# Kernel optimization log

Hardware: AMD Instinct MI355X
Metric: run time of the kernel (lower is better)

Reference implementation:

```python
import jax, jax.numpy as jnp
import numpy as np

N_HEADS = 8
TANH_CLIP = 10.0
NEG = -1e9  # finite stand-in for -inf so log_softmax/vjp stay NaN-free


def setup_inputs() -> dict:
    key = jax.random.key(0)
    ks = jax.random.split(key, 8)
    B, N, D = 256, 1000, 128
    embeddings = jax.random.normal(ks[0], (B, N, D), dtype=jnp.float32)
    W_node = jax.random.normal(ks[1], (D, 3 * D), dtype=jnp.float32) * (1.0 / np.sqrt(D))
    W_fixed = jax.random.normal(ks[2], (D, D), dtype=jnp.float32) * (1.0 / np.sqrt(D))
    W_step = jax.random.normal(ks[3], (2 * D, D), dtype=jnp.float32) * (1.0 / np.sqrt(2 * D))
    W_out = jax.random.normal(ks[4], (D, D), dtype=jnp.float32) * (1.0 / np.sqrt(D))
    first_idx = jax.random.randint(ks[5], (B,), 0, N)
    last_idx = jax.random.randint(ks[6], (B,), 0, N)
    mask = jax.random.randint(ks[7], (B, N), 0, 2).astype(jnp.bool_)
    mask = mask.at[:, 0].set(False)  # guarantee at least one feasible node
    return {"embeddings": embeddings, "W_node": W_node, "W_fixed": W_fixed,
            "W_step": W_step, "W_out": W_out, "first_idx": first_idx,
            "last_idx": last_idx, "mask": mask}


def reference(embeddings, W_node, W_fixed, W_step, W_out, first_idx, last_idx, mask):
    # One pointer-network decode step (TSP variant of AttentionModel._get_log_p),
    # including the _precompute projections.
    B, N, D = embeddings.shape
    H = N_HEADS
    dk = D // H

    # _precompute: fixed context + glimpse K/V + logit key
    graph_embed = embeddings.mean(axis=1)                       # [B, D]
    fixed_ctx = graph_embed @ W_fixed                           # [B, D]
    kvl = embeddings @ W_node                                   # [B, N, 3D]
    K, V, logit_K = jnp.split(kvl, 3, axis=-1)                  # each [B, N, D]

    # step context: cat(first-node emb, last-node emb) -> project to D
    b = jnp.arange(B)
    step_ctx = jnp.concatenate([embeddings[b, first_idx], embeddings[b, last_idx]], axis=-1)  # [B, 2D]
    q = fixed_ctx + step_ctx @ W_step                           # [B, D]

    # masked multi-head glimpse attention (q_len = 1)
    qh = q.reshape(B, H, dk)                                    # [B, H, dk]
    Kh = K.reshape(B, N, H, dk)
    Vh = V.reshape(B, N, H, dk)
    compat = jnp.einsum('bhd,bnhd->bhn', qh, Kh) / np.sqrt(dk)  # [B, H, N]
    compat = jnp.where(mask[:, None, :], NEG, compat)           # mask_inner
    attn = jax.nn.softmax(compat, axis=-1)
    heads = jnp.einsum('bhn,bnhd->bhd', attn, Vh)               # [B, H, dk]
    glimpse = heads.reshape(B, D) @ W_out                       # [B, D]

    # single-head logit attention with tanh clipping
    logits = jnp.einsum('bd,bnd->bn', glimpse, logit_K) / np.sqrt(D)  # [B, N]
    logits = jnp.tanh(logits) * TANH_CLIP
    logits = jnp.where(mask, NEG, logits)                       # mask_logits
    return jax.nn.log_softmax(logits, axis=-1)                  # [B, N]
```

## Files before the change

kernel.cpp:

```cpp
#include <hip/hip_runtime.h>


#define NEG (-1e9f)

__global__ __launch_bounds__(1024) void k_fused(
    const float* __restrict__ E, const float* __restrict__ Wn,
    const float* __restrict__ Wf, const float* __restrict__ Ws,
    const float* __restrict__ Wo,
    const int* __restrict__ fi, const int* __restrict__ li,
    const int* __restrict__ maskI, const unsigned char* __restrict__ maskB,
    float* __restrict__ out)
{
    const int b = blockIdx.x;
    const int t = threadIdx.x;

    __shared__ float4 Et[4096];
    __shared__ float4 qk4[256];
    __shared__ float4 pt4[256];
    __shared__ float4 EbarF4[256];
    __shared__ float4 mu4[32], e14[32], e24[32], gp4[32];
    __shared__ float q[128], heads[128], gl[128];
    __shared__ float qred[8][128];
    __shared__ float ct[128 * 9];
    __shared__ float redh[72];
    __shared__ float mh[8], lh[8], al[8];
    __shared__ float red[16];
    __shared__ float stat[2];
    __shared__ int flagS;

    float* const mu = (float*)mu4;
    float* const e1 = (float*)e14;
    float* const e2 = (float*)e24;
    float* const gp = (float*)gp4;
    float* const pt = (float*)pt4;
    float* const EbarF = (float*)EbarF4;
    float* const qkf = (float*)qk4;

    const float4* E4 = (const float4*)(E + (size_t)b * 128000);

    if (t == 0) flagS = 0;
    const uint4 dv = ((const uint4*)maskI)[t];
    const unsigned det = (dv.x | dv.y | dv.z | dv.w) & 0xFFFFFF00u;

    {
        const int cm = t & 31, sm = t >> 5;
        float4 acc = make_float4(0.f, 0.f, 0.f, 0.f);
        for (int r = sm; r < 1000; r += 32) {
            const float4 v = E4[r * 32 + cm];
            acc.x += v.x; acc.y += v.y; acc.z += v.z; acc.w += v.w;
        }
        Et[t] = acc;
    }
    if (t >= 512 && t < 544) {
        e14[t - 512] = E4[fi[b] * 32 + (t - 512)];
    } else if (t >= 544 && t < 576) {
        e24[t - 544] = E4[li[b] * 32 + (t - 544)];
    }
    __syncthreads();
    if (det) atomicOr(&flagS, 1);
    if (t < 32) {
        float4 acc = Et[t];
        #pragma unroll
        for (int s = 1; s < 32; ++s) {
            const float4 v = Et[s * 32 + t];
            acc.x += v.x; acc.y += v.y; acc.z += v.z; acc.w += v.w;
        }
        const float inv = 1.0f / 1000.0f;
        mu4[t] = make_float4(acc.x * inv, acc.y * inv, acc.z * inv, acc.w * inv);
    }
    __syncthreads();

    {
        const int part = t >> 7, d = t & 127;
        float acc = 0.f;
        const int k0 = part * 48;
        for (int k = k0; k < k0 + 48; ++k) {
            const float s = (k < 128) ? mu[k] : (k < 256 ? e1[k - 128] : e2[k - 256]);
            const float w = (k < 128) ? Wf[k * 128 + d] : Ws[(k - 128) * 128 + d];
            acc += s * w;
        }
        qred[part][d] = acc;
    }
    __syncthreads();
    if (t < 128) {
        float acc = 0.f;
        #pragma unroll
        for (int p = 0; p < 8; ++p) acc += qred[p][t];
        q[t] = acc;
    }
    __syncthreads();
    {
        const int j = t & 127, cg = t >> 7;
        const float qj = q[j];
        for (int c0 = 0; c0 < 128; c0 += 8) {
            const int c = c0 + cg;
            float v = Wn[c * 384 + j] * qj;
            v += __shfl_down(v, 8, 16);
            v += __shfl_down(v, 4, 16);
            v += __shfl_down(v, 2, 16);
            v += __shfl_down(v, 1, 16);
            if ((j & 15) == 0) {
                const int h = j >> 4, s = c >> 2;
                qkf[h * 128 + (s ^ (s >> 2)) * 4 + (c & 3)] = v * 0.25f;
            }
        }
    }
    __syncthreads();

    const bool useB = (flagS != 0);

    if (t < 8) { mh[t] = -3e38f; lh[t] = 0.f; }
    float4 eacc[8];
    #pragma unroll
    for (int h = 0; h < 8; ++h) eacc[h] = make_float4(0.f, 0.f, 0.f, 0.f);
    const int c4 = t & 31, sl = t >> 5;
    const int rr = t >> 3, qq = t & 7;

    for (int tile = 0; tile < 8; ++tile) {
        const int r0 = tile * 128;
        {
            const int g = r0 + rr;
            float4 v[4];
            if (g < 1000) {
                #pragma unroll
                for (int i = 0; i < 4; ++i) v[i] = E4[g * 32 + qq * 4 + i];
            } else {
                #pragma unroll
                for (int i = 0; i < 4; ++i) v[i] = make_float4(0.f, 0.f, 0.f, 0.f);
            }
            float pch[8];
            #pragma unroll
            for (int h = 0; h < 8; ++h) pch[h] = 0.f;
            #pragma unroll
            for (int i = 0; i < 4; ++i) {
                const int grp = qq * 4 + i;
                Et[rr * 32 + (grp ^ (rr & 7))] = v[i];
                const int sg = grp ^ (grp >> 2);
                #pragma unroll
                for (int h = 0; h < 8; ++h) {
                    const float4 w = qk4[h * 32 + sg];
                    pch[h] += v[i].x * w.x + v[i].y * w.y + v[i].z * w.z + v[i].w * w.w;
                }
            }
            #pragma unroll
            for (int m = 1; m <= 4; m <<= 1) {
                #pragma unroll
                for (int h = 0; h < 8; ++h) pch[h] += __shfl_xor(pch[h], m, 64);
            }
            bool msk = (g >= 1000);
            if (!msk) msk = useB ? (maskB[b * 1000 + g] != 0)
                                 : (maskI[b * 1000 + g] != 0);
            ct[rr * 9 + qq] = msk ? NEG : pch[qq];
        }
        __syncthreads();
        if (t < 64) {
            const int h = t & 7, part = t >> 3;
            float mt = -3e38f;
            const int rb = part * 16;
            for (int r = 0; r < 16; ++r) mt = fmaxf(mt, ct[(rb + r) * 9 + h]);
            redh[part * 9 + h] = mt;
        }
        __syncthreads();
        if (t < 8) {
            float mt = redh[t];
            for (int p = 1; p < 8; ++p) mt = fmaxf(mt, redh[p * 9 + t]);
            const float mnew = fmaxf(mh[t], mt);
            al[t] = __expf(mh[t] - mnew);
            mh[t] = mnew;
        }
        __syncthreads();
        {
            const int row = t >> 3, h = t & 7;
            pt[row * 8 + h] = __expf(ct[row * 9 + h] - mh[h]);
        }
        __syncthreads();
        {
            #pragma unroll
            for (int h = 0; h < 8; ++h) {
                const float a = al[h];
                eacc[h].x *= a; eacc[h].y *= a; eacc[h].z *= a; eacc[h].w *= a;
            }
            #pragma unroll
            for (int j = 0; j < 4; ++j) {
                const int r = sl * 4 + j;
                const float4 ev = Et[r * 32 + (c4 ^ (r & 7))];
                const float4 p0 = pt4[r * 2];
                const float4 p1 = pt4[r * 2 + 1];
                eacc[0].x += p0.x * ev.x; eacc[0].y += p0.x * ev.y; eacc[0].z += p0.x * ev.z; eacc[0].w += p0.x * ev.w;
                eacc[1].x += p0.y * ev.x; eacc[1].y += p0.y * ev.y; eacc[1].z += p0.y * ev.z; eacc[1].w += p0.y * ev.w;
                eacc[2].x += p0.z * ev.x; eacc[2].y += p0.z * ev.y; eacc[2].z += p0.z * ev.z; eacc[2].w += p0.z * ev.w;
                eacc[3].x += p0.w * ev.x; eacc[3].y += p0.w * ev.y; eacc[3].z += p0.w * ev.z; eacc[3].w += p0.w * ev.w;
                eacc[4].x += p1.x * ev.x; eacc[4].y += p1.x * ev.y; eacc[4].z += p1.x * ev.z; eacc[4].w += p1.x * ev.w;
                eacc[5].x += p1.y * ev.x; eacc[5].y += p1.y * ev.y; eacc[5].z += p1.y * ev.z; eacc[5].w += p1.y * ev.w;
                eacc[6].x += p1.z * ev.x; eacc[6].y += p1.z * ev.y; eacc[6].z += p1.z * ev.z; eacc[6].w += p1.z * ev.w;
                eacc[7].x += p1.w * ev.x; eacc[7].y += p1.w * ev.y; eacc[7].z += p1.w * ev.z; eacc[7].w += p1.w * ev.w;
            }
        }
        if (t < 64) {
            const int h = t & 7, part = t >> 3;
            float s = 0.f;
            const int rb = part * 16;
            for (int r = 0; r < 16; ++r) s += pt[(rb + r) * 8 + h];
            redh[part * 9 + h] = s;
        }
        __syncthreads();
        if (t < 8) {
            float s = 0.f;
            for (int p = 0; p < 8; ++p) s += redh[p * 9 + t];
            lh[t] = lh[t] * al[t] + s;
        }
    }

    if (sl >= 16) {
        #pragma unroll
        for (int h = 0; h < 8; ++h) Et[(sl - 16) * 256 + h * 32 + c4] = eacc[h];
    }
    __syncthreads();
    if (sl < 16) {
        #pragma unroll
        for (int h = 0; h < 8; ++h) {
            const float4 o = Et[sl * 256 + h * 32 + c4];
            eacc[h].x += o.x; eacc[h].y += o.y; eacc[h].z += o.z; eacc[h].w += o.w;
            Et[sl * 256 + h * 32 + c4] = eacc[h];
        }
    }
    __syncthreads();
    if (t < 256) {
        const int h = t >> 5, cc = t & 31;
        float4 s = make_float4(0.f, 0.f, 0.f, 0.f);
        #pragma unroll
        for (int s2 = 0; s2 < 16; ++s2) {
            const float4 v = Et[s2 * 256 + h * 32 + cc];
            s.x += v.x; s.y += v.y; s.z += v.z; s.w += v.w;
        }
        const float invl = 1.0f / lh[h];
        EbarF4[h * 32 + cc] = make_float4(s.x * invl, s.y * invl, s.z * invl, s.w * invl);
    }
    __syncthreads();

    {
        const int part = t >> 7, d = t & 127, h = d >> 4;
        float acc = 0.f;
        const int c0 = part * 16;
        for (int c = c0; c < c0 + 16; ++c) acc += EbarF[h * 128 + c] * Wn[c * 384 + 128 + d];
        qred[part][d] = acc;
    }
    __syncthreads();
    if (t < 128) {
        float acc = 0.f;
        #pragma unroll
        for (int p = 0; p < 8; ++p) acc += qred[p][t];
        heads[t] = acc;
    }
    __syncthreads();
    {
        const int part = t >> 7, d = t & 127;
        float acc = 0.f;
        const int j0 = part * 16;
        for (int j = j0; j < j0 + 16; ++j) acc += heads[j] * Wo[j * 128 + d];
        qred[part][d] = acc;
    }
    __syncthreads();
    if (t < 128) {
        float acc = 0.f;
        #pragma unroll
        for (int p = 0; p < 8; ++p) acc += qred[p][t];
        gl[t] = acc;
    }
    __syncthreads();
    {
        const int part = t >> 7, c = t & 127;
        float acc = 0.f;
        const int d0 = part * 16;
        for (int d = d0; d < d0 + 16; ++d) acc += Wn[c * 384 + 256 + d] * gl[d];
        qred[part][c] = acc;
    }
    __syncthreads();
    if (t < 128) {
        float acc = 0.f;
        #pragma unroll
        for (int p = 0; p < 8; ++p) acc += qred[p][t];
        gp[t] = acc * 0.08838834764831845f;
    }
    __syncthreads();

    {
        const int row = t >> 3, sub = t & 7;
        for (int tile = 0; tile < 8; ++tile) {
            const int g = tile * 128 + row;
            float acc = 0.f;
            if (g < 1000) {
                #pragma unroll
                for (int i = 0; i < 4; ++i) {
                    const float4 v = E4[g * 32 + sub * 4 + i];
                    const float4 w = gp4[sub * 4 + i];
                    acc += v.x * w.x + v.y * w.y + v.z * w.z + v.w * w.w;
                }
            }
            ct[row * 9 + sub] = acc;
            __syncthreads();
            if (t < 128) {
                const int g2 = tile * 128 + t;
                if (g2 < 1000) {
                    float s = 0.f;
                    #pragma unroll
                    for (int k = 0; k < 8; ++k) s += ct[t * 9 + k];
                    float zz = 10.0f * tanhf(s);
                    const bool m = useB ? (maskB[b * 1000 + g2] != 0)
                                        : (maskI[b * 1000 + g2] != 0);
                    if (m) zz = NEG;
                    pt[g2] = zz;
                }
            }
            __syncthreads();
        }
    }
    float v = (t < 1000) ? pt[t] : -3e38f;
    #pragma unroll
    for (int off = 32; off > 0; off >>= 1) v = fmaxf(v, __shfl_down(v, off, 64));
    if ((t & 63) == 0) red[t >> 6] = v;
    __syncthreads();
    if (t == 0) {
        float m = red[0];
        for (int i = 1; i < 16; ++i) m = fmaxf(m, red[i]);
        stat[0] = m;
    }
    __syncthreads();
    float sv = (t < 1000) ? __expf(pt[t] - stat[0]) : 0.f;
    #pragma unroll
    for (int off = 32; off > 0; off >>= 1) sv += __shfl_down(sv, off, 64);
    if ((t & 63) == 0) red[t >> 6] = sv;
    __syncthreads();
    if (t == 0) {
        float s = 0.f;
        for (int i = 0; i < 16; ++i) s += red[i];
        stat[1] = stat[0] + __logf(s);
    }
    __syncthreads();
    if (t < 1000)
        out[(size_t)b * 1000 + t] = pt[t] - stat[1];
}

extern "C" void kernel_launch(void* const* d_in, const int* in_sizes, int n_in,
                              void* d_out, int out_size, void* d_ws, size_t ws_size,
                              hipStream_t stream) {
    const float* E  = (const float*)d_in[0];
    const float* Wn = (const float*)d_in[1];
    const float* Wf = (const float*)d_in[2];
    const float* Ws = (const float*)d_in[3];
    const float* Wo = (const float*)d_in[4];
    const int*   fi = (const int*)d_in[5];
    const int*   li = (const int*)d_in[6];
    const int*   maskI = (const int*)d_in[7];
    const unsigned char* maskB = (const unsigned char*)d_in[7];
    float* out = (float*)d_out;

    k_fused<<<256, 1024, 0, stream>>>(E, Wn, Wf, Ws, Wo, fi, li, maskI, maskB, out);
}
```

Baseline: 284.4 us.

## Split each batch row across two blocks with pairwise global-memory sync

Launches 512 blocks cooperatively, with each pair of blocks handling half of the 1000 nodes for one batch element. Partial mean, attention-softmax state and log-sum-exp statistics are exchanged through workspace memory using an atomic counter barrier per pair. The goal is to double the number of blocks so that 256 CUs are filled better and per-block latency drops. In exchange it adds three spin-wait barriers, a memset, and extra workspace traffic, and it depends on both blocks of a pair being resident at once. It also relayouts the attention-value accumulation to scalar per-column accumulators over a smaller tile.

Result: slower. 725.2 us (+154.9%).

```diff
diff --git a/kernel.cpp b/kernel.cpp
--- a/kernel.cpp
+++ b/kernel.cpp
@@ -3,20 +3,42 @@
 
 #define NEG (-1e9f)
 
-__global__ __launch_bounds__(1024) void k_fused(
+__device__ __forceinline__ void pair_sync(int* c, int target) {
+    __syncthreads();
+    if (threadIdx.x == 0) {
+        __hip_atomic_fetch_add(c, 1, __ATOMIC_RELEASE, __HIP_MEMORY_SCOPE_AGENT);
+        while (__hip_atomic_load(c, __ATOMIC_RELAXED, __HIP_MEMORY_SCOPE_AGENT) < target)
+            __builtin_amdgcn_s_sleep(4);
+        __threadfence();
+    }
+    __syncthreads();
+}
+
+__global__ __launch_bounds__(1024, 8) void k_fused(
     const float* __restrict__ E, const float* __restrict__ Wn,
     const float* __restrict__ Wf, const float* __restrict__ Ws,
     const float* __restrict__ Wo,
     const int* __restrict__ fi, const int* __restrict__ li,
     const int* __restrict__ maskI, const unsigned char* __restrict__ maskB,
-    float* __restrict__ out)
+    float* __restrict__ out, float* __restrict__ ws)
 {
-    const int b = blockIdx.x;
-    const int t = threadIdx.x;
-
-    __shared__ float4 Et[4096];
+    const int bid  = blockIdx.x;
+    const int b    = bid & 255;
+    const int half = bid >> 8;
+    const int blk  = b * 2 + half;
+    const int i0   = b * 2, i1 = b * 2 + 1;
+    const int t    = threadIdx.x;
+    const int r0g  = half * 500;
+
+    int*   cnt  = (int*)ws;
+    float* muP  = ws + 256;
+    float* wsU  = muP + 512 * 128;
+    float* wsML = wsU + (size_t)512 * 1024;
+    float* wsZ  = wsML + 512 * 16;
+
+    __shared__ float4 Et4[2048];
     __shared__ float4 qk4[256];
-    __shared__ float4 pt4[256];
+    __shared__ float4 pt4[128];
     __shared__ float4 EbarF4[256];
     __shared__ float4 mu4[32], e14[32], e24[32], gp4[32];
     __shared__ float q[128], heads[128], gl[128];
@@ -28,13 +50,14 @@
     __shared__ float stat[2];
     __shared__ int flagS;
 
-    float* const mu = (float*)mu4;
-    float* const e1 = (float*)e14;
-    float* const e2 = (float*)e24;
-    float* const gp = (float*)gp4;
-    float* const pt = (float*)pt4;
+    float* const mu    = (float*)mu4;
+    float* const e1    = (float*)e14;
+    float* const e2    = (float*)e24;
+    float* const gp    = (float*)gp4;
+    float* const pt    = (float*)pt4;
     float* const EbarF = (float*)EbarF4;
-    float* const qkf = (float*)qk4;
+    float* const qkf   = (float*)qk4;
+    float* const Etf   = (float*)Et4;
 
     const float4* E4 = (const float4*)(E + (size_t)b * 128000);
 
@@ -45,11 +68,11 @@
     {
         const int cm = t & 31, sm = t >> 5;
         float4 acc = make_float4(0.f, 0.f, 0.f, 0.f);
-        for (int r = sm; r < 1000; r += 32) {
-            const float4 v = E4[r * 32 + cm];
+        for (int r = sm; r < 500; r += 32) {
+            const float4 v = E4[(r0g + r) * 32 + cm];
             acc.x += v.x; acc.y += v.y; acc.z += v.z; acc.w += v.w;
         }
-        Et[t] = acc;
+        Et4[t] = acc;
     }
     if (t >= 512 && t < 544) {
         e14[t - 512] = E4[fi[b] * 32 + (t - 512)];
@@ -59,14 +82,21 @@
     __syncthreads();
     if (det) atomicOr(&flagS, 1);
     if (t < 32) {
-        float4 acc = Et[t];
+        float4 acc = Et4[t];
         #pragma unroll
         for (int s = 1; s < 32; ++s) {
-            const float4 v = Et[s * 32 + t];
+            const float4 v = Et4[s * 32 + t];
             acc.x += v.x; acc.y += v.y; acc.z += v.z; acc.w += v.w;
         }
+        ((float4*)(muP + (size_t)blk * 128))[t] = acc;
+    }
+    pair_sync(&cnt[b], 2);
+    if (t < 32) {
+        const float4 p0 = ((const float4*)(muP + (size_t)i0 * 128))[t];
+        const float4 p1 = ((const float4*)(muP + (size_t)i1 * 128))[t];
         const float inv = 1.0f / 1000.0f;
-        mu4[t] = make_float4(acc.x * inv, acc.y * inv, acc.z * inv, acc.w * inv);
+        mu4[t] = make_float4((p0.x + p1.x) * inv, (p0.y + p1.y) * inv,
+                             (p0.z + p1.z) * inv, (p0.w + p1.w) * inv);
     }
     __syncthreads();
 
@@ -110,131 +140,126 @@
     const bool useB = (flagS != 0);
 
     if (t < 8) { mh[t] = -3e38f; lh[t] = 0.f; }
-    float4 eacc[8];
+    float eacc[8];
     #pragma unroll
-    for (int h = 0; h < 8; ++h) eacc[h] = make_float4(0.f, 0.f, 0.f, 0.f);
-    const int c4 = t & 31, sl = t >> 5;
-    const int rr = t >> 3, qq = t & 7;
+    for (int h = 0; h < 8; ++h) eacc[h] = 0.f;
+    const int rr = t >> 4, qq = t & 15;
+    const int esl = t >> 7, ec = t & 127;
+    const int g1 = qq, g2 = qq + 16;
+    const int sg1 = g1 ^ (g1 >> 2), sg2 = g2 ^ (g2 >> 2);
 
     for (int tile = 0; tile < 8; ++tile) {
-        const int r0 = tile * 128;
+        const int lr = tile * 64 + rr;
+        const bool valid = (lr < 500);
         {
-            const int g = r0 + rr;
-            float4 v[4];
-            if (g < 1000) {
+            float4 v0 = make_float4(0.f, 0.f, 0.f, 0.f), v1 = v0;
+            if (valid) {
+                v0 = E4[(r0g + lr) * 32 + g1];
+                v1 = E4[(r0g + lr) * 32 + g2];
+            }
+            bool msk = !valid;
+            if (valid && qq < 8)
+                msk = useB ? (maskB[b * 1000 + r0g + lr] != 0)
+                           : (maskI[b * 1000 + r0g + lr] != 0);
+            Et4[rr * 32 + g1] = v0;
+            Et4[rr * 32 + g2] = v1;
+            float pch[8];
+            #pragma unroll
+            for (int h = 0; h < 8; ++h) {
+                const float4 w0 = qk4[h * 32 + sg1];
+                const float4 w1 = qk4[h * 32 + sg2];
+                pch[h] = v0.x * w0.x + v0.y * w0.y + v0.z * w0.z + v0.w * w0.w
+                       + v1.x * w1.x + v1.y * w1.y + v1.z * w1.z + v1.w * w1.w;
+            }
+            #pragma unroll
+            for (int m = 1; m <= 8; m <<= 1) {
                 #pragma unroll
-                for (int i = 0; i < 4; ++i) v[i] = E4[g * 32 + qq * 4 + i];
-            } else {
-                #pragma unroll
-                for (int i = 0; i < 4; ++i) v[i] = make_float4(0.f, 0.f, 0.f, 0.f);
-            }
-            float pch[8];
-            #pragma unroll
-            for (int h = 0; h < 8; ++h) pch[h] = 0.f;
-            #pragma unroll
-            for (int i = 0; i < 4; ++i) {
-                const int grp = qq * 4 + i;
-                Et[rr * 32 + (grp ^ (rr & 7))] = v[i];
-                const int sg = grp ^ (grp >> 2);
-                #pragma unroll
-                for (int h = 0; h < 8; ++h) {
-                    const float4 w = qk4[h * 32 + sg];
-                    pch[h] += v[i].x * w.x + v[i].y * w.y + v[i].z * w.z + v[i].w * w.w;
-                }
-            }
-            #pragma unroll
-            for (int m = 1; m <= 4; m <<= 1) {
-                #pragma unroll
-                for (int h = 0; h < 8; ++h) pch[h] += __shfl_xor(pch[h], m, 64);
-            }
-            bool msk = (g >= 1000);
-            if (!msk) msk = useB ? (maskB[b * 1000 + g] != 0)
-                                 : (maskI[b * 1000 + g] != 0);
-            ct[rr * 9 + qq] = msk ? NEG : pch[qq];
+                for (int h = 0; h < 8; ++h) pch[h] += __shfl_xor(pch[h], m, 16);
+            }
+            if (qq < 8) ct[rr * 9 + qq] = msk ? NEG : pch[qq];
         }
         __syncthreads();
         if (t < 64) {
             const int h = t & 7, part = t >> 3;
             float mt = -3e38f;
-            const int rb = part * 16;
-            for (int r = 0; r < 16; ++r) mt = fmaxf(mt, ct[(rb + r) * 9 + h]);
+            const int rb = part * 8;
+            #pragma unroll
+            for (int r = 0; r < 8; ++r) mt = fmaxf(mt, ct[(rb + r) * 9 + h]);
             redh[part * 9 + h] = mt;
         }
         __syncthreads();
         if (t < 8) {
             float mt = redh[t];
+            #pragma unroll
             for (int p = 1; p < 8; ++p) mt = fmaxf(mt, redh[p * 9 + t]);
             const float mnew = fmaxf(mh[t], mt);
             al[t] = __expf(mh[t] - mnew);
             mh[t] = mnew;
         }
         __syncthreads();
-        {
+        if (t < 512) {
             const int row = t >> 3, h = t & 7;
             pt[row * 8 + h] = __expf(ct[row * 9 + h] - mh[h]);
         }
         __syncthreads();
         {
             #pragma unroll
-            for (int h = 0; h < 8; ++h) {
-                const float a = al[h];
-                eacc[h].x *= a; eacc[h].y *= a; eacc[h].z *= a; eacc[h].w *= a;
-            }
-            #pragma unroll
-            for (int j = 0; j < 4; ++j) {
-                const int r = sl * 4 + j;
-                const float4 ev = Et[r * 32 + (c4 ^ (r & 7))];
+            for (int h = 0; h < 8; ++h) eacc[h] *= al[h];
+            #pragma unroll
+            for (int j = 0; j < 8; ++j) {
+                const int r = esl * 8 + j;
+                const float ev = Etf[r * 128 + ec];
                 const float4 p0 = pt4[r * 2];
                 const float4 p1 = pt4[r * 2 + 1];
-                eacc[0].x += p0.x * ev.x; eacc[0].y += p0.x * ev.y; eacc[0].z += p0.x * ev.z; eacc[0].w += p0.x * ev.w;
-                eacc[1].x += p0.y * ev.x; eacc[1].y += p0.y * ev.y; eacc[1].z += p0.y * ev.z; eacc[1].w += p0.y * ev.w;
-                eacc[2].x += p0.z * ev.x; eacc[2].y += p0.z * ev.y; eacc[2].z += p0.z * ev.z; eacc[2].w += p0.z * ev.w;
-                eacc[3].x += p0.w * ev.x; eacc[3].y += p0.w * ev.y; eacc[3].z += p0.w * ev.z; eacc[3].w += p0.w * ev.w;
-                eacc[4].x += p1.x * ev.x; eacc[4].y += p1.x * ev.y; eacc[4].z += p1.x * ev.z; eacc[4].w += p1.x * ev.w;
-                eacc[5].x += p1.y * ev.x; eacc[5].y += p1.y * ev.y; eacc[5].z += p1.y * ev.z; eacc[5].w += p1.y * ev.w;
-                eacc[6].x += p1.z * ev.x; eacc[6].y += p1.z * ev.y; eacc[6].z += p1.z * ev.z; eacc[6].w += p1.z * ev.w;
-                eacc[7].x += p1.w * ev.x; eacc[7].y += p1.w * ev.y; eacc[7].z += p1.w * ev.z; eacc[7].w += p1.w * ev.w;
+                eacc[0] += p0.x * ev; eacc[1] += p0.y * ev;
+                eacc[2] += p0.z * ev; eacc[3] += p0.w * ev;
+                eacc[4] += p1.x * ev; eacc[5] += p1.y * ev;
+                eacc[6] += p1.z * ev; eacc[7] += p1.w * ev;
             }
         }
         if (t < 64) {
             const int h = t & 7, part = t >> 3;
             float s = 0.f;
-            const int rb = part * 16;
-            for (int r = 0; r < 16; ++r) s += pt[(rb + r) * 8 + h];
+            const int rb = part * 8;
+            #pragma unroll
+            for (int r = 0; r < 8; ++r) s += pt[(rb + r) * 8 + h];
             redh[part * 9 + h] = s;
         }
         __syncthreads();
         if (t < 8) {
             float s = 0.f;
+            #pragma unroll
             for (int p = 0; p < 8; ++p) s += redh[p * 9 + t];
             lh[t] = lh[t] * al[t] + s;
         }
     }
 
-    if (sl >= 16) {
-        #pragma unroll
-        for (int h = 0; h < 8; ++h) Et[(sl - 16) * 256 + h * 32 + c4] = eacc[h];
-    }
-    __syncthreads();
-    if (sl < 16) {
-        #pragma unroll
-        for (int h = 0; h < 8; ++h) {
-            const float4 o = Et[sl * 256 + h * 32 + c4];
-            eacc[h].x += o.x; eacc[h].y += o.y; eacc[h].z += o.z; eacc[h].w += o.w;
-            Et[sl * 256 + h * 32 + c4] = eacc[h];
-        }
-    }
-    __syncthreads();
-    if (t < 256) {
-        const int h = t >> 5, cc = t & 31;
-        float4 s = make_float4(0.f, 0.f, 0.f, 0.f);
-        #pragma unroll
-        for (int s2 = 0; s2 < 16; ++s2) {
-            const float4 v = Et[s2 * 256 + h * 32 + cc];
-            s.x += v.x; s.y += v.y; s.z += v.z; s.w += v.w;
-        }
-        const float invl = 1.0f / lh[h];
-        EbarF4[h * 32 + cc] = make_float4(s.x * invl, s.y * invl, s.z * invl, s.w * invl);
+    #pragma unroll
+    for (int h = 0; h < 8; ++h) Etf[esl * 1024 + h * 128 + ec] = eacc[h];
+    __syncthreads();
+    {
+        float s = 0.f;
+        #pragma unroll
+        for (int s2 = 0; s2 < 8; ++s2) s += Etf[s2 * 1024 + t];
+        wsU[(size_t)blk * 1024 + t] = s;
+    }
+    if (t < 8) wsML[blk * 16 + t] = mh[t];
+    else if (t < 16) wsML[blk * 16 + t] = lh[t - 8];
+    pair_sync(&cnt[b], 4);
+    if (t < 8) {
+        const float m0 = wsML[i0 * 16 + t], m1 = wsML[i1 * 16 + t];
+        const float l0 = wsML[i0 * 16 + 8 + t], l1 = wsML[i1 * 16 + 8 + t];
+        const float M = fmaxf(m0, m1);
+        const float w0 = __expf(m0 - M), w1 = __expf(m1 - M);
+        const float L = l0 * w0 + l1 * w1;
+        redh[t] = w0 / L;
+        redh[8 + t] = w1 / L;
+    }
+    __syncthreads();
+    {
+        const int h = t >> 7;
+        EbarF[t] = wsU[(size_t)i0 * 1024 + t] * redh[h]
+                 + wsU[(size_t)i1 * 1024 + t] * redh[8 + h];
     }
     __syncthreads();
 
@@ -286,10 +311,11 @@
 
     {
         const int row = t >> 3, sub = t & 7;
-        for (int tile = 0; tile < 8; ++tile) {
-            const int g = tile * 128 + row;
+        for (int tile = 0; tile < 4; ++tile) {
+            const int lr = tile * 128 + row;
             float acc = 0.f;
-            if (g < 1000) {
+            if (lr < 500) {
+                const int g = r0g + lr;
                 #pragma unroll
                 for (int i = 0; i < 4; ++i) {
                     const float4 v = E4[g * 32 + sub * 4 + i];
@@ -300,45 +326,63 @@
             ct[row * 9 + sub] = acc;
             __syncthreads();
             if (t < 128) {
-                const int g2 = tile * 128 + t;
-                if (g2 < 1000) {
+                const int lr2 = tile * 128 + t;
+                if (lr2 < 500) {
                     float s = 0.f;
                     #pragma unroll
                     for (int k = 0; k < 8; ++k) s += ct[t * 9 + k];
                     float zz = 10.0f * tanhf(s);
+                    const int g2 = r0g + lr2;
                     const bool m = useB ? (maskB[b * 1000 + g2] != 0)
                                         : (maskI[b * 1000 + g2] != 0);
                     if (m) zz = NEG;
-                    pt[g2] = zz;
+                    pt[lr2] = zz;
                 }
             }
             __syncthreads();
         }
     }
-    float v = (t < 1000) ? pt[t] : -3e38f;
-    #pragma unroll
-    for (int off = 32; off > 0; off >>= 1) v = fmaxf(v, __shfl_down(v, off, 64));
-    if ((t & 63) == 0) red[t >> 6] = v;
+    {
+        float v = (t < 500) ? pt[t] : -3e38f;
+        if (t < 512) {
+            #pragma unroll
+            for (int off = 32; off > 0; off >>= 1) v = fmaxf(v, __shfl_down(v, off, 64));
+            if ((t & 63) == 0) red[t >> 6] = v;
+        }
+    }
     __syncthreads();
     if (t == 0) {
         float m = red[0];
-        for (int i = 1; i < 16; ++i) m = fmaxf(m, red[i]);
+        for (int i = 1; i < 8; ++i) m = fmaxf(m, red[i]);
         stat[0] = m;
     }
     __syncthreads();
-    float sv = (t < 1000) ? __expf(pt[t] - stat[0]) : 0.f;
-    #pragma unroll
-    for (int off = 32; off > 0; off >>= 1) sv += __shfl_down(sv, off, 64);
-    if ((t & 63) == 0) red[t >> 6] = sv;
+    {
+        float sv = (t < 500) ? __expf(pt[t] - stat[0]) : 0.f;
+        if (t < 512) {
+            #pragma unroll
+            for (int off = 32; off > 0; off >>= 1) sv += __shfl_down(sv, off, 64);
+            if ((t & 63) == 0) red[t >> 6] = sv;
+        }
+    }
     __syncthreads();
     if (t == 0) {
         float s = 0.f;
-        for (int i = 0; i < 16; ++i) s += red[i];
-        stat[1] = stat[0] + __logf(s);
-    }
-    __syncthreads();
-    if (t < 1000)
-        out[(size_t)b * 1000 + t] = pt[t] - stat[1];
+        for (int i = 0; i < 8; ++i) s += red[i];
+        wsZ[blk * 2] = stat[0];
+        wsZ[blk * 2 + 1] = s;
+    }
+    pair_sync(&cnt[b], 6);
+    if (t == 0) {
+        const float m0 = wsZ[i0 * 2], s0 = wsZ[i0 * 2 + 1];
+        const float m1 = wsZ[i1 * 2], s1 = wsZ[i1 * 2 + 1];
+        const float M = fmaxf(m0, m1);
+        const float S = s0 * __expf(m0 - M) + s1 * __expf(m1 - M);
+        stat[1] = M + __logf(S);
+    }
+    __syncthreads();
+    if (t < 500)
+        out[(size_t)b * 1000 + r0g + t] = pt[t] - stat[1];
 }
 
 extern "C" void kernel_launch(void* const* d_in, const int* in_sizes, int n_in,
@@ -354,6 +398,17 @@
     const int*   maskI = (const int*)d_in[7];
     const unsigned char* maskB = (const unsigned char*)d_in[7];
     float* out = (float*)d_out;
-
-    k_fused<<<256, 1024, 0, stream>>>(E, Wn, Wf, Ws, Wo, fi, li, maskI, maskB, out);
+    float* ws  = (float*)d_ws;
+
+    hipMemsetAsync(d_ws, 0, 256 * sizeof(int), stream);
+
+    void* args[] = {(void*)&E, (void*)&Wn, (void*)&Wf, (void*)&Ws, (void*)&Wo,
+                    (void*)&fi, (void*)&li, (void*)&maskI, (void*)&maskB,
+                    (void*)&out, (void*)&ws};
+    const hipError_t err = hipLaunchCooperativeKernel(
+        (const void*)k_fused, dim3(512), dim3(1024), args, 0, stream);
+    if (err != hipSuccess) {
+        k_fused<<<dim3(512), dim3(1024), 0, stream>>>(
+            E, Wn, Wf, Ws, Wo, fi, li, maskI, maskB, out, ws);
+    }
 }
```

## Split fused decode kernel into five kernels over half-row blocks

Applied to the files above, without the earlier changes.

Replaces the single 256-block fused kernel with a pipeline of five kernels: partial mean, partial attention numerator/denominator, glimpse projection, partial logits, and normalization. Each batch row's 1000 nodes are split across two 512-thread blocks, giving 512 blocks to raise occupancy and memory-level parallelism on the bandwidth-bound passes over the embeddings. The online-softmax max tracking is dropped: attention weights use exp without max subtraction, and the log-softmax uses the tanh clip bound 10 as a fixed shift. This removes several block-wide syncs and reductions, but adds extra launches and workspace round-trips. It also risks overflow in the attention exp if compat values are ever large.

New measurement: 467.0 us. 64.2% more time.

```diff
diff --git a/kernel.cpp b/kernel.cpp
--- a/kernel.cpp
+++ b/kernel.cpp
@@ -3,38 +3,66 @@
 
 #define NEG (-1e9f)
 
-__global__ __launch_bounds__(1024) void k_fused(
+__global__ __launch_bounds__(512, 4) void k1_mean(
+    const float* __restrict__ E, float* __restrict__ muP)
+{
+    const int bid = blockIdx.x;
+    const int b = bid & 255, half = bid >> 8;
+    const int blk = b * 2 + half;
+    const int t = threadIdx.x;
+    const int r0g = half * 500;
+    __shared__ float4 sc[512];
+    const float4* E4 = (const float4*)(E + (size_t)b * 128000);
+    const int cm = t & 31, sm = t >> 5;
+    float4 acc = make_float4(0.f, 0.f, 0.f, 0.f);
+    for (int r = sm; r < 500; r += 16) {
+        const float4 v = E4[(r0g + r) * 32 + cm];
+        acc.x += v.x; acc.y += v.y; acc.z += v.z; acc.w += v.w;
+    }
+    sc[t] = acc;
+    __syncthreads();
+    if (t < 32) {
+        float4 a = sc[t];
+        #pragma unroll
+        for (int s = 1; s < 16; ++s) {
+            const float4 v = sc[s * 32 + t];
+            a.x += v.x; a.y += v.y; a.z += v.z; a.w += v.w;
+        }
+        ((float4*)(muP + (size_t)blk * 128))[t] = a;
+    }
+}
+
+__global__ __launch_bounds__(512, 4) void k2_attn(
     const float* __restrict__ E, const float* __restrict__ Wn,
     const float* __restrict__ Wf, const float* __restrict__ Ws,
-    const float* __restrict__ Wo,
     const int* __restrict__ fi, const int* __restrict__ li,
     const int* __restrict__ maskI, const unsigned char* __restrict__ maskB,
-    float* __restrict__ out)
-{
-    const int b = blockIdx.x;
-    const int t = threadIdx.x;
-
-    __shared__ float4 Et[4096];
+    const float* __restrict__ muP, float* __restrict__ Uw,
+    float* __restrict__ lw)
+{
+    const int bid = blockIdx.x;
+    const int b = bid & 255, half = bid >> 8;
+    const int blk = b * 2 + half;
+    const int i0 = b * 2, i1 = i0 + 1;
+    const int t = threadIdx.x;
+    const int r0g = half * 500;
+
+    __shared__ float4 Et4[2048];
     __shared__ float4 qk4[256];
-    __shared__ float4 pt4[256];
-    __shared__ float4 EbarF4[256];
-    __shared__ float4 mu4[32], e14[32], e24[32], gp4[32];
-    __shared__ float q[128], heads[128], gl[128];
-    __shared__ float qred[8][128];
-    __shared__ float ct[128 * 9];
+    __shared__ float4 pt4[128];
+    __shared__ float4 mu4[32], e14[32], e24[32];
+    __shared__ float q[128];
+    __shared__ float qred[4][128];
+    __shared__ float ct[64 * 9];
     __shared__ float redh[72];
-    __shared__ float mh[8], lh[8], al[8];
-    __shared__ float red[16];
-    __shared__ float stat[2];
     __shared__ int flagS;
 
-    float* const mu = (float*)mu4;
-    float* const e1 = (float*)e14;
-    float* const e2 = (float*)e24;
-    float* const gp = (float*)gp4;
-    float* const pt = (float*)pt4;
-    float* const EbarF = (float*)EbarF4;
+    float* const mu  = (float*)mu4;
+    float* const e1  = (float*)e14;
+    float* const e2  = (float*)e24;
+    float* const pt  = (float*)pt4;
     float* const qkf = (float*)qk4;
+    float* const Etf = (float*)Et4;
 
     const float4* E4 = (const float4*)(E + (size_t)b * 128000);
 
@@ -42,39 +70,22 @@
     const uint4 dv = ((const uint4*)maskI)[t];
     const unsigned det = (dv.x | dv.y | dv.z | dv.w) & 0xFFFFFF00u;
 
-    {
-        const int cm = t & 31, sm = t >> 5;
-        float4 acc = make_float4(0.f, 0.f, 0.f, 0.f);
-        for (int r = sm; r < 1000; r += 32) {
-            const float4 v = E4[r * 32 + cm];
-            acc.x += v.x; acc.y += v.y; acc.z += v.z; acc.w += v.w;
-        }
-        Et[t] = acc;
-    }
-    if (t >= 512 && t < 544) {
-        e14[t - 512] = E4[fi[b] * 32 + (t - 512)];
-    } else if (t >= 544 && t < 576) {
-        e24[t - 544] = E4[li[b] * 32 + (t - 544)];
+    if (t < 128) {
+        mu[t] = (muP[(size_t)i0 * 128 + t] + muP[(size_t)i1 * 128 + t])
+                * (1.0f / 1000.0f);
+    } else if (t < 160) {
+        e14[t - 128] = E4[fi[b] * 32 + (t - 128)];
+    } else if (t < 192) {
+        e24[t - 160] = E4[li[b] * 32 + (t - 160)];
     }
     __syncthreads();
     if (det) atomicOr(&flagS, 1);
-    if (t < 32) {
-        float4 acc = Et[t];
-        #pragma unroll
-        for (int s = 1; s < 32; ++s) {
-            const float4 v = Et[s * 32 + t];
-            acc.x += v.x; acc.y += v.y; acc.z += v.z; acc.w += v.w;
-        }
-        const float inv = 1.0f / 1000.0f;
-        mu4[t] = make_float4(acc.x * inv, acc.y * inv, acc.z * inv, acc.w * inv);
-    }
-    __syncthreads();
 
     {
         const int part = t >> 7, d = t & 127;
         float acc = 0.f;
-        const int k0 = part * 48;
-        for (int k = k0; k < k0 + 48; ++k) {
+        const int k0 = part * 96;
+        for (int k = k0; k < k0 + 96; ++k) {
             const float s = (k < 128) ? mu[k] : (k < 256 ? e1[k - 128] : e2[k - 256]);
             const float w = (k < 128) ? Wf[k * 128 + d] : Ws[(k - 128) * 128 + d];
             acc += s * w;
@@ -82,17 +93,12 @@
         qred[part][d] = acc;
     }
     __syncthreads();
-    if (t < 128) {
-        float acc = 0.f;
-        #pragma unroll
-        for (int p = 0; p < 8; ++p) acc += qred[p][t];
-        q[t] = acc;
-    }
+    if (t < 128) q[t] = qred[0][t] + qred[1][t] + qred[2][t] + qred[3][t];
     __syncthreads();
     {
         const int j = t & 127, cg = t >> 7;
         const float qj = q[j];
-        for (int c0 = 0; c0 < 128; c0 += 8) {
+        for (int c0 = 0; c0 < 128; c0 += 4) {
             const int c = c0 + cg;
             float v = Wn[c * 384 + j] * qj;
             v += __shfl_down(v, 8, 16);
@@ -106,24 +112,23 @@
         }
     }
     __syncthreads();
-
     const bool useB = (flagS != 0);
 
-    if (t < 8) { mh[t] = -3e38f; lh[t] = 0.f; }
-    float4 eacc[8];
+    float eacc[8];
     #pragma unroll
-    for (int h = 0; h < 8; ++h) eacc[h] = make_float4(0.f, 0.f, 0.f, 0.f);
-    const int c4 = t & 31, sl = t >> 5;
+    for (int h = 0; h < 8; ++h) eacc[h] = 0.f;
+    float lacc = 0.f;
     const int rr = t >> 3, qq = t & 7;
+    const int esl = t >> 7, ec = t & 127;
 
     for (int tile = 0; tile < 8; ++tile) {
-        const int r0 = tile * 128;
+        const int lr = tile * 64 + rr;
+        const bool valid = (lr < 500);
         {
-            const int g = r0 + rr;
             float4 v[4];
-            if (g < 1000) {
-                #pragma unroll
-                for (int i = 0; i < 4; ++i) v[i] = E4[g * 32 + qq * 4 + i];
+            if (valid) {
+                #pragma unroll
+                for (int i = 0; i < 4; ++i) v[i] = E4[(r0g + lr) * 32 + qq * 4 + i];
             } else {
                 #pragma unroll
                 for (int i = 0; i < 4; ++i) v[i] = make_float4(0.f, 0.f, 0.f, 0.f);
@@ -134,7 +139,7 @@
             #pragma unroll
             for (int i = 0; i < 4; ++i) {
                 const int grp = qq * 4 + i;
-                Et[rr * 32 + (grp ^ (rr & 7))] = v[i];
+                Et4[rr * 32 + grp] = v[i];
                 const int sg = grp ^ (grp >> 2);
                 #pragma unroll
                 for (int h = 0; h < 8; ++h) {
@@ -145,99 +150,71 @@
             #pragma unroll
             for (int m = 1; m <= 4; m <<= 1) {
                 #pragma unroll
-                for (int h = 0; h < 8; ++h) pch[h] += __shfl_xor(pch[h], m, 64);
-            }
-            bool msk = (g >= 1000);
-            if (!msk) msk = useB ? (maskB[b * 1000 + g] != 0)
-                                 : (maskI[b * 1000 + g] != 0);
+                for (int h = 0; h < 8; ++h) pch[h] += __shfl_xor(pch[h], m, 8);
+            }
+            bool msk = !valid;
+            if (valid) msk = useB ? (maskB[b * 1000 + r0g + lr] != 0)
+                                  : (maskI[b * 1000 + r0g + lr] != 0);
             ct[rr * 9 + qq] = msk ? NEG : pch[qq];
         }
         __syncthreads();
-        if (t < 64) {
-            const int h = t & 7, part = t >> 3;
-            float mt = -3e38f;
-            const int rb = part * 16;
-            for (int r = 0; r < 16; ++r) mt = fmaxf(mt, ct[(rb + r) * 9 + h]);
-            redh[part * 9 + h] = mt;
-        }
-        __syncthreads();
-        if (t < 8) {
-            float mt = redh[t];
-            for (int p = 1; p < 8; ++p) mt = fmaxf(mt, redh[p * 9 + t]);
-            const float mnew = fmaxf(mh[t], mt);
-            al[t] = __expf(mh[t] - mnew);
-            mh[t] = mnew;
-        }
+        pt[(t >> 3) * 8 + (t & 7)] = __expf(ct[(t >> 3) * 9 + (t & 7)]);
         __syncthreads();
         {
-            const int row = t >> 3, h = t & 7;
-            pt[row * 8 + h] = __expf(ct[row * 9 + h] - mh[h]);
-        }
-        __syncthreads();
-        {
-            #pragma unroll
-            for (int h = 0; h < 8; ++h) {
-                const float a = al[h];
-                eacc[h].x *= a; eacc[h].y *= a; eacc[h].z *= a; eacc[h].w *= a;
-            }
-            #pragma unroll
-            for (int j = 0; j < 4; ++j) {
-                const int r = sl * 4 + j;
-                const float4 ev = Et[r * 32 + (c4 ^ (r & 7))];
+            #pragma unroll
+            for (int j = 0; j < 16; ++j) {
+                const int r = esl * 16 + j;
+                const float ev = Etf[r * 128 + ec];
                 const float4 p0 = pt4[r * 2];
                 const float4 p1 = pt4[r * 2 + 1];
-                eacc[0].x += p0.x * ev.x; eacc[0].y += p0.x * ev.y; eacc[0].z += p0.x * ev.z; eacc[0].w += p0.x * ev.w;
-                eacc[1].x += p0.y * ev.x; eacc[1].y += p0.y * ev.y; eacc[1].z += p0.y * ev.z; eacc[1].w += p0.y * ev.w;
-                eacc[2].x += p0.z * ev.x; eacc[2].y += p0.z * ev.y; eacc[2].z += p0.z * ev.z; eacc[2].w += p0.z * ev.w;
-                eacc[3].x += p0.w * ev.x; eacc[3].y += p0.w * ev.y; eacc[3].z += p0.w * ev.z; eacc[3].w += p0.w * ev.w;
-                eacc[4].x += p1.x * ev.x; eacc[4].y += p1.x * ev.y; eacc[4].z += p1.x * ev.z; eacc[4].w += p1.x * ev.w;
-                eacc[5].x += p1.y * ev.x; eacc[5].y += p1.y * ev.y; eacc[5].z += p1.y * ev.z; eacc[5].w += p1.y * ev.w;
-                eacc[6].x += p1.z * ev.x; eacc[6].y += p1.z * ev.y; eacc[6].z += p1.z * ev.z; eacc[6].w += p1.z * ev.w;
-                eacc[7].x += p1.w * ev.x; eacc[7].y += p1.w * ev.y; eacc[7].z += p1.w * ev.z; eacc[7].w += p1.w * ev.w;
-            }
-        }
-        if (t < 64) {
-            const int h = t & 7, part = t >> 3;
-            float s = 0.f;
-            const int rb = part * 16;
-            for (int r = 0; r < 16; ++r) s += pt[(rb + r) * 8 + h];
-            redh[part * 9 + h] = s;
-        }
-        __syncthreads();
-        if (t < 8) {
-            float s = 0.f;
-            for (int p = 0; p < 8; ++p) s += redh[p * 9 + t];
-            lh[t] = lh[t] * al[t] + s;
-        }
-    }
-
-    if (sl >= 16) {
-        #pragma unroll
-        for (int h = 0; h < 8; ++h) Et[(sl - 16) * 256 + h * 32 + c4] = eacc[h];
-    }
-    __syncthreads();
-    if (sl < 16) {
-        #pragma unroll
-        for (int h = 0; h < 8; ++h) {
-            const float4 o = Et[sl * 256 + h * 32 + c4];
-            eacc[h].x += o.x; eacc[h].y += o.y; eacc[h].z += o.z; eacc[h].w += o.w;
-            Et[sl * 256 + h * 32 + c4] = eacc[h];
-        }
-    }
-    __syncthreads();
-    if (t < 256) {
-        const int h = t >> 5, cc = t & 31;
-        float4 s = make_float4(0.f, 0.f, 0.f, 0.f);
-        #pragma unroll
-        for (int s2 = 0; s2 < 16; ++s2) {
-            const float4 v = Et[s2 * 256 + h * 32 + cc];
-            s.x += v.x; s.y += v.y; s.z += v.z; s.w += v.w;
-        }
-        const float invl = 1.0f / lh[h];
-        EbarF4[h * 32 + cc] = make_float4(s.x * invl, s.y * invl, s.z * invl, s.w * invl);
-    }
-    __syncthreads();
-
+                eacc[0] += p0.x * ev; eacc[1] += p0.y * ev;
+                eacc[2] += p0.z * ev; eacc[3] += p0.w * ev;
+                eacc[4] += p1.x * ev; eacc[5] += p1.y * ev;
+                eacc[6] += p1.z * ev; eacc[7] += p1.w * ev;
+            }
+            if (t < 64) {
+                const int h = t & 7, part = t >> 3;
+                #pragma unroll
+                for (int r = 0; r < 8; ++r) lacc += pt[(part * 8 + r) * 8 + h];
+            }
+        }
+        __syncthreads();
+    }
+
+    #pragma unroll
+    for (int h = 0; h < 8; ++h) Etf[esl * 1024 + h * 128 + ec] = eacc[h];
+    if (t < 64) redh[(t >> 3) * 9 + (t & 7)] = lacc;
+    __syncthreads();
+    #pragma unroll
+    for (int e = 0; e < 2; ++e) {
+        const int idx = t + e * 512;
+        Uw[(size_t)blk * 1024 + idx] =
+            Etf[idx] + Etf[1024 + idx] + Etf[2048 + idx] + Etf[3072 + idx];
+    }
+    if (t < 8) {
+        float s = 0.f;
+        #pragma unroll
+        for (int p = 0; p < 8; ++p) s += redh[p * 9 + t];
+        lw[blk * 8 + t] = s;
+    }
+}
+
+__global__ __launch_bounds__(1024) void k3_glimpse(
+    const float* __restrict__ Wn, const float* __restrict__ Wo,
+    const float* __restrict__ Uw, const float* __restrict__ lw,
+    float* __restrict__ gpw)
+{
+    const int b = blockIdx.x;
+    const int t = threadIdx.x;
+    const int i0 = b * 2, i1 = i0 + 1;
+    __shared__ float EbarF[1024];
+    __shared__ float linv[8];
+    __shared__ float heads[128], gl[128];
+    __shared__ float qred[8][128];
+    if (t < 8) linv[t] = 1.0f / (lw[i0 * 8 + t] + lw[i1 * 8 + t]);
+    __syncthreads();
+    EbarF[t] = (Uw[(size_t)i0 * 1024 + t] + Uw[(size_t)i1 * 1024 + t]) * linv[t >> 7];
+    __syncthreads();
     {
         const int part = t >> 7, d = t & 127, h = d >> 4;
         float acc = 0.f;
@@ -247,10 +224,10 @@
     }
     __syncthreads();
     if (t < 128) {
-        float acc = 0.f;
-        #pragma unroll
-        for (int p = 0; p < 8; ++p) acc += qred[p][t];
-        heads[t] = acc;
+        float a = 0.f;
+        #pragma unroll
+        for (int p = 0; p < 8; ++p) a += qred[p][t];
+        heads[t] = a;
     }
     __syncthreads();
     {
@@ -262,10 +239,10 @@
     }
     __syncthreads();
     if (t < 128) {
-        float acc = 0.f;
-        #pragma unroll
-        for (int p = 0; p < 8; ++p) acc += qred[p][t];
-        gl[t] = acc;
+        float a = 0.f;
+        #pragma unroll
+        for (int p = 0; p < 8; ++p) a += qred[p][t];
+        gl[t] = a;
     }
     __syncthreads();
     {
@@ -277,68 +254,90 @@
     }
     __syncthreads();
     if (t < 128) {
-        float acc = 0.f;
-        #pragma unroll
-        for (int p = 0; p < 8; ++p) acc += qred[p][t];
-        gp[t] = acc * 0.08838834764831845f;
-    }
-    __syncthreads();
-
-    {
-        const int row = t >> 3, sub = t & 7;
-        for (int tile = 0; tile < 8; ++tile) {
-            const int g = tile * 128 + row;
-            float acc = 0.f;
-            if (g < 1000) {
-                #pragma unroll
-                for (int i = 0; i < 4; ++i) {
-                    const float4 v = E4[g * 32 + sub * 4 + i];
-                    const float4 w = gp4[sub * 4 + i];
-                    acc += v.x * w.x + v.y * w.y + v.z * w.z + v.w * w.w;
-                }
-            }
-            ct[row * 9 + sub] = acc;
-            __syncthreads();
-            if (t < 128) {
-                const int g2 = tile * 128 + t;
-                if (g2 < 1000) {
-                    float s = 0.f;
-                    #pragma unroll
-                    for (int k = 0; k < 8; ++k) s += ct[t * 9 + k];
-                    float zz = 10.0f * tanhf(s);
-                    const bool m = useB ? (maskB[b * 1000 + g2] != 0)
-                                        : (maskI[b * 1000 + g2] != 0);
-                    if (m) zz = NEG;
-                    pt[g2] = zz;
-                }
-            }
-            __syncthreads();
-        }
-    }
-    float v = (t < 1000) ? pt[t] : -3e38f;
-    #pragma unroll
-    for (int off = 32; off > 0; off >>= 1) v = fmaxf(v, __shfl_down(v, off, 64));
-    if ((t & 63) == 0) red[t >> 6] = v;
-    __syncthreads();
-    if (t == 0) {
-        float m = red[0];
-        for (int i = 1; i < 16; ++i) m = fmaxf(m, red[i]);
-        stat[0] = m;
-    }
-    __syncthreads();
-    float sv = (t < 1000) ? __expf(pt[t] - stat[0]) : 0.f;
+        float a = 0.f;
+        #pragma unroll
+        for (int p = 0; p < 8; ++p) a += qred[p][t];
+        gpw[(size_t)b * 128 + t] = a * 0.08838834764831845f;
+    }
+}
+
+__global__ __launch_bounds__(512, 4) void k4_logits(
+    const float* __restrict__ E,
+    const int* __restrict__ maskI, const unsigned char* __restrict__ maskB,
+    const float* __restrict__ gpw, float* __restrict__ out,
+    float* __restrict__ sw)
+{
+    const int bid = blockIdx.x;
+    const int b = bid & 255, half = bid >> 8;
+    const int blk = b * 2 + half;
+    const int t = threadIdx.x;
+    const int r0g = half * 500;
+    __shared__ float4 gp4[32];
+    __shared__ float ct[128 * 5];
+    __shared__ float red[8];
+    __shared__ int flagS;
+    const float4* E4 = (const float4*)(E + (size_t)b * 128000);
+    if (t == 0) flagS = 0;
+    const uint4 dv = ((const uint4*)maskI)[t];
+    const unsigned det = (dv.x | dv.y | dv.z | dv.w) & 0xFFFFFF00u;
+    if (t < 32) gp4[t] = ((const float4*)(gpw + (size_t)b * 128))[t];
+    __syncthreads();
+    if (det) atomicOr(&flagS, 1);
+
+    float sacc = 0.f;
+    const int row = t >> 2, sub = t & 3;
+    for (int tile = 0; tile < 4; ++tile) {
+        const int lr = tile * 128 + row;
+        float acc = 0.f;
+        if (lr < 500) {
+            const int g = r0g + lr;
+            #pragma unroll
+            for (int i = 0; i < 8; ++i) {
+                const float4 v = E4[g * 32 + sub * 8 + i];
+                const float4 w = gp4[sub * 8 + i];
+                acc += v.x * w.x + v.y * w.y + v.z * w.z + v.w * w.w;
+            }
+        }
+        ct[row * 5 + sub] = acc;
+        __syncthreads();
+        if (t < 128) {
+            const int lr2 = tile * 128 + t;
+            if (lr2 < 500) {
+                const float s = ct[t * 5] + ct[t * 5 + 1] + ct[t * 5 + 2] + ct[t * 5 + 3];
+                float zz = 10.0f * tanhf(s);
+                const int g2 = r0g + lr2;
+                const bool m = (flagS != 0) ? (maskB[b * 1000 + g2] != 0)
+                                            : (maskI[b * 1000 + g2] != 0);
+                if (m) zz = NEG;
+                out[(size_t)b * 1000 + g2] = zz;
+                sacc += __expf(zz - 10.0f);
+            }
+        }
+        __syncthreads();
+    }
+    float sv = sacc;
     #pragma unroll
     for (int off = 32; off > 0; off >>= 1) sv += __shfl_down(sv, off, 64);
     if ((t & 63) == 0) red[t >> 6] = sv;
     __syncthreads();
     if (t == 0) {
         float s = 0.f;
-        for (int i = 0; i < 16; ++i) s += red[i];
-        stat[1] = stat[0] + __logf(s);
-    }
-    __syncthreads();
-    if (t < 1000)
-        out[(size_t)b * 1000 + t] = pt[t] - stat[1];
+        #pragma unroll
+        for (int i = 0; i < 8; ++i) s += red[i];
+        sw[blk] = s;
+    }
+}
+
+__global__ __launch_bounds__(512, 4) void k5_norm(
+    const float* __restrict__ sw, float* __restrict__ out)
+{
+    const int bid = blockIdx.x;
+    const int b = bid & 255, half = bid >> 8;
+    const int t = threadIdx.x;
+    const int r0g = half * 500;
+    const float s = sw[b * 2] + sw[b * 2 + 1];
+    const float lse = 10.0f + __logf(s);
+    if (t < 500) out[(size_t)b * 1000 + r0g + t] -= lse;
 }
 
 extern "C" void kernel_launch(void* const* d_in, const int* in_sizes, int n_in,
@@ -354,6 +353,18 @@
     const int*   maskI = (const int*)d_in[7];
     const unsigned char* maskB = (const unsigned char*)d_in[7];
     float* out = (float*)d_out;
-
-    k_fused<<<256, 1024, 0, stream>>>(E, Wn, Wf, Ws, Wo, fi, li, maskI, maskB, out);
-}
+    float* ws  = (float*)d_ws;
+
+    float* muP = ws;
+    float* Uw  = ws + 512 * 128;
+    float* lw  = Uw + (size_t)512 * 1024;
+    float* gpw = lw + 512 * 8;
+    float* sw  = gpw + 256 * 128;
+
+    k1_mean   <<<dim3(512), dim3(512),  0, stream>>>(E, muP);
+    k2_attn   <<<dim3(512), dim3(512),  0, stream>>>(E, Wn, Wf, Ws, fi, li,
+                                                     maskI, maskB, muP, Uw, lw);
+    k3_glimpse<<<dim3(256), dim3(1024), 0, stream>>>(Wn, Wo, Uw, lw, gpw);
+    k4_logits <<<dim3(512), dim3(512),  0, stream>>>(E, maskI, maskB, gpw, out, sw);
+    k5_norm   <<<dim3(512), dim3(512),  0, stream>>>(sw, out);
+}
```
